# Kernel optimization log

Measured on AMD Instinct MI355X. Metric: run time of the kernel, lower is better.

## Reference

```python
import jax, jax.numpy as jnp
import numpy as np

B, C, INTER, T, H, W = 2, 256, 64, 8, 32, 32


def setup_inputs() -> dict:
    key = jax.random.key(0)
    ks = jax.random.split(key, 4)
    scale_q = 1.0 / np.sqrt(C)
    x = jax.random.normal(ks[0], (B, C, T, H, W), dtype=jnp.float32)
    Wq = jax.random.normal(ks[1], (INTER, C), dtype=jnp.float32) * scale_q
    Wk = jax.random.normal(ks[2], (INTER, C), dtype=jnp.float32) * scale_q
    Wv = jax.random.normal(ks[3], (C, C), dtype=jnp.float32) * scale_q
    return {
        "x": x,
        "Wq": Wq, "bq": jnp.zeros((INTER,), jnp.float32),
        "Wk": Wk, "bk": jnp.zeros((INTER,), jnp.float32),
        "Wv": Wv, "bv": jnp.zeros((C,), jnp.float32),
    }


def reference(x, Wq, bq, Wk, bk, Wv, bv):
    b, c, t, h, w = x.shape
    n = t * h * w
    xf = x.reshape(b, c, n)  # [B, C, N] (row-major flatten over T,H,W)
    # 1x1x1 Conv3d == per-voxel linear projection
    q = jnp.einsum('oc,bcn->bno', Wq, xf) + bq          # [B, N, INTER]
    k = jnp.einsum('oc,bcn->bon', Wk, xf) + bk[:, None]  # [B, INTER, N]
    v = jnp.einsum('oc,bcn->bon', Wv, xf) + bv[:, None]  # [B, C, N]
    energy = jnp.einsum('bid,bdj->bij', q, k)            # [B, N, N]
    attention = jax.nn.softmax(energy, axis=-1)
    # out[b,c,i] = sum_j v[b,c,j] * attention[b,i,j]
    out = jnp.einsum('bcj,bij->bci', v, attention)       # [B, C, N]
    out = out.reshape(b, c, t, h, w) + x
    return out
```

## Files before the change

### kernel.cpp

```cpp
#include <hip/hip_runtime.h>
#include <hip/hip_bf16.h>

typedef short short8 __attribute__((ext_vector_type(8)));
typedef float float4v __attribute__((ext_vector_type(4)));

#define MFMA(a, b, c) __builtin_amdgcn_mfma_f32_16x16x32_bf16((a), (b), (c), 0, 0, 0)

typedef const __attribute__((address_space(1))) unsigned int gu32;
typedef __attribute__((address_space(3))) unsigned int lu32;
#define GLOAD_LDS16(g, l) __builtin_amdgcn_global_load_lds((gu32*)(g), (lu32*)(l), 16, 0, 0)

#define LOG2E 1.4426950408889634f

static __device__ __forceinline__ unsigned short f2bf(float f) {
    union { float f; unsigned u; } v; v.f = f;
    unsigned r = (v.u + 0x7fffu + ((v.u >> 16) & 1u)) >> 16;
    return (unsigned short)r;
}
static __device__ __forceinline__ float bf2f(unsigned short h) {
    union { unsigned u; float f; } v; v.u = ((unsigned)h) << 16;
    return v.f;
}
static __device__ __forceinline__ unsigned pk2bf(float a, float b) {
    union { __hip_bfloat162 h; unsigned u; } cv;
    cv.h = __float22bfloat162_rn(make_float2(a, b));
    return cv.u;
}

static __device__ __forceinline__ int qk_idx(int b, int n, int o) {
    int frag = (b * 512 + (n >> 4)) * 2 + (o >> 5);
    return frag * 512 + ((o >> 3) & 3) * 128 + (n & 15) * 8 + (o & 7);
}
static __device__ __forceinline__ int v_idx(int b, int c, int n) {
    int frag = (b * 256 + (n >> 5)) * 16 + (c >> 4);
    return frag * 512 + ((n >> 3) & 3) * 128 + (c & 15) * 8 + (n & 7);
}

__global__ void wcvt(const float* __restrict__ Wq, const float* __restrict__ Wk,
                     const float* __restrict__ Wv,
                     unsigned short* __restrict__ Whi, unsigned short* __restrict__ Wlo) {
    int idx = blockIdx.x * 256 + threadIdx.x;
    if (idx >= 384 * 256) return;
    int row = idx >> 8, c = idx & 255;
    float f;
    if (row < 64)       f = Wq[row * 256 + c];
    else if (row < 128) f = Wk[(row - 64) * 256 + c];
    else                f = Wv[(row - 128) * 256 + c];
    unsigned short hi = f2bf(f);
    Whi[idx] = hi;
    if (row < 128) Wlo[idx] = f2bf(f - bf2f(hi));
}

__global__ __launch_bounds__(256, 1) void proj(
        const float* __restrict__ x, const unsigned short* __restrict__ Whi,
        const unsigned short* __restrict__ Wlo,
        const float* __restrict__ bq, const float* __restrict__ bk,
        const float* __restrict__ bv,
        unsigned short* __restrict__ qhi_ws, unsigned short* __restrict__ qlo_ws,
        unsigned short* __restrict__ khi_ws, unsigned short* __restrict__ klo_ws,
        unsigned short* __restrict__ vws) {
    __shared__ unsigned short XThi[64 * 264];
    __shared__ unsigned short XTlo[64 * 264];

    const int tid = threadIdx.x;
    const int b  = blockIdx.x >> 7;
    const int n0 = (blockIdx.x & 127) << 6;
    const float* xb = x + b * 2097152;

    for (int p = 0; p < 16; ++p) {
        int idx = p * 256 + tid;
        int c = idx >> 4, nq = idx & 15;
        float4v xv = *reinterpret_cast<const float4v*>(xb + c * 8192 + n0 + nq * 4);
#pragma unroll
        for (int q = 0; q < 4; ++q) {
            unsigned short hi = f2bf(xv[q]);
            XThi[(nq * 4 + q) * 264 + c] = hi;
            XTlo[(nq * 4 + q) * 264 + c] = f2bf(xv[q] - bf2f(hi));
        }
    }
    __syncthreads();

    const int lane = tid & 63, w = tid >> 6;
    const int quad = lane >> 4, l16 = lane & 15;

    short8 aXhi[8], aXlo[8];
#pragma unroll
    for (int ks = 0; ks < 8; ++ks) {
        aXhi[ks] = *reinterpret_cast<const short8*>(&XThi[(w * 16 + l16) * 264 + ks * 32 + quad * 8]);
        aXlo[ks] = *reinterpret_cast<const short8*>(&XTlo[(w * 16 + l16) * 264 + ks * 32 + quad * 8]);
    }

#pragma unroll
    for (int ot = 0; ot < 8; ++ot) {
        float4v acc = {0.f, 0.f, 0.f, 0.f};
#pragma unroll
        for (int ks = 0; ks < 8; ++ks) {
            short8 bwhi = *reinterpret_cast<const short8*>(&Whi[(ot * 16 + l16) * 256 + ks * 32 + quad * 8]);
            short8 bwlo = *reinterpret_cast<const short8*>(&Wlo[(ot * 16 + l16) * 256 + ks * 32 + quad * 8]);
            acc = MFMA(aXhi[ks], bwhi, acc);
            acc = MFMA(aXlo[ks], bwhi, acc);
            acc = MFMA(aXhi[ks], bwlo, acc);
        }
        int o = ot * 16 + l16;
        float bias = (ot < 4) ? bq[o] : bk[o - 64];
#pragma unroll
        for (int r = 0; r < 4; ++r) {
            int n = n0 + w * 16 + quad * 4 + r;
            float y = acc[r] + bias;
            if (ot < 4) y *= LOG2E;
            unsigned short hi = f2bf(y);
            unsigned short lo = f2bf(y - bf2f(hi));
            if (ot < 4) {
                int id = qk_idx(b, n, o);
                qhi_ws[id] = hi; qlo_ws[id] = lo;
            } else {
                int id = qk_idx(b, n, o - 64);
                khi_ws[id] = hi; klo_ws[id] = lo;
            }
        }
    }

    float4v acc2[4][4];
#pragma unroll
    for (int mt = 0; mt < 4; ++mt)
#pragma unroll
        for (int nt = 0; nt < 4; ++nt) acc2[mt][nt] = (float4v){0.f, 0.f, 0.f, 0.f};

#pragma unroll
    for (int ks = 0; ks < 8; ++ks) {
        short8 aW[4], bX[4];
#pragma unroll
        for (int mt = 0; mt < 4; ++mt)
            aW[mt] = *reinterpret_cast<const short8*>(&Whi[(128 + w * 64 + mt * 16 + l16) * 256 + ks * 32 + quad * 8]);
#pragma unroll
        for (int nt = 0; nt < 4; ++nt)
            bX[nt] = *reinterpret_cast<const short8*>(&XThi[(nt * 16 + l16) * 264 + ks * 32 + quad * 8]);
#pragma unroll
        for (int mt = 0; mt < 4; ++mt)
#pragma unroll
            for (int nt = 0; nt < 4; ++nt)
                acc2[mt][nt] = MFMA(aW[mt], bX[nt], acc2[mt][nt]);
    }
#pragma unroll
    for (int mt = 0; mt < 4; ++mt) {
#pragma unroll
        for (int r = 0; r < 4; ++r) {
            int c = w * 64 + mt * 16 + quad * 4 + r;
            float bias = bv[c];
#pragma unroll
            for (int nt = 0; nt < 4; ++nt) {
                int n = n0 + nt * 16 + l16;
                vws[v_idx(b, c, n)] = f2bf(acc2[mt][nt][r] + bias);
            }
        }
    }
}

__global__ __launch_bounds__(256, 2) void attn(
        const unsigned short* __restrict__ qhi_ws, const unsigned short* __restrict__ qlo_ws,
        const unsigned short* __restrict__ khi_ws, const unsigned short* __restrict__ klo_ws,
        const unsigned short* __restrict__ vws,
        unsigned short* __restrict__ Opart, float* __restrict__ ml) {
    __shared__ unsigned short Vlds[3][8192];
    __shared__ unsigned short Pl[4 * 32 * 36];

    const int tid = threadIdx.x, lane = tid & 63, w = tid >> 6;
    const int quad = lane >> 4, l16 = lane & 15;
    const int xcd = blockIdx.x & 7, b = xcd & 1, jr = xcd >> 1;
    const int it = blockIdx.x >> 3;
    const int iw16 = it * 8 + w * 2;
    unsigned short* Pw = Pl + w * (32 * 36);

    const unsigned short* khb = khi_ws + (size_t)((b * 512 + jr * 128) * 2) * 512 + lane * 8;
    const unsigned short* klb = klo_ws + (size_t)((b * 512 + jr * 128) * 2) * 512 + lane * 8;
    const unsigned short* qhb = qhi_ws + (size_t)((b * 512 + iw16) * 2) * 512 + lane * 8;
    const unsigned short* qlb = qlo_ws + (size_t)((b * 512 + iw16) * 2) * 512 + lane * 8;
    const unsigned short* vstage = vws + ((size_t)(b * 256 + jr * 64) * 16 + w * 4) * 512 + lane * 8;

    short8 qh[2][2], ql[2][2];
#pragma unroll
    for (int mt = 0; mt < 2; ++mt)
#pragma unroll
        for (int kf = 0; kf < 2; ++kf) {
            qh[mt][kf] = *reinterpret_cast<const short8*>(qhb + (mt * 2 + kf) * 512);
            ql[mt][kf] = *reinterpret_cast<const short8*>(qlb + (mt * 2 + kf) * 512);
        }

    float4v acc[2][16];
#pragma unroll
    for (int mt = 0; mt < 2; ++mt)
#pragma unroll
        for (int cf = 0; cf < 16; ++cf) acc[mt][cf] = (float4v){0.f, 0.f, 0.f, 0.f};
    float lrow[2][4];
    short8 aP[2];
#pragma unroll
    for (int mt = 0; mt < 2; ++mt)
#pragma unroll
        for (int r = 0; r < 4; ++r) lrow[mt][r] = 0.f;

#pragma unroll
    for (int q = 0; q < 4; ++q)
        GLOAD_LDS16(vstage + q * 512, &Vlds[0][(w * 4 + q) * 512]);
    vstage += 8192;

    int bprev = 2, bcur = 0, bnext = 1;
#pragma unroll 1
    for (int itn = 0; itn < 64; ++itn) {
        if (itn) __syncthreads();

        if (itn < 63) {
#pragma unroll
            for (int q = 0; q < 4; ++q)
                GLOAD_LDS16(vstage + q * 512, &Vlds[bnext][(w * 4 + q) * 512]);
            vstage += 8192;
        }

        float4v s[2][2];
#pragma unroll
        for (int mt = 0; mt < 2; ++mt)
#pragma unroll
            for (int jt = 0; jt < 2; ++jt) s[mt][jt] = (float4v){0.f, 0.f, 0.f, 0.f};
#pragma unroll
        for (int jt = 0; jt < 2; ++jt) {
            short8 kh0 = *reinterpret_cast<const short8*>(khb + (jt * 2 + 0) * 512);
            short8 kh1 = *reinterpret_cast<const short8*>(khb + (jt * 2 + 1) * 512);
            short8 kl0 = *reinterpret_cast<const short8*>(klb + (jt * 2 + 0) * 512);
            short8 kl1 = *reinterpret_cast<const short8*>(klb + (jt * 2 + 1) * 512);
#pragma unroll
            for (int mt = 0; mt < 2; ++mt) {
                s[mt][jt] = MFMA(qh[mt][0], kh0, s[mt][jt]);
                s[mt][jt] = MFMA(ql[mt][0], kh0, s[mt][jt]);
                s[mt][jt] = MFMA(qh[mt][0], kl0, s[mt][jt]);
                s[mt][jt] = MFMA(qh[mt][1], kh1, s[mt][jt]);
                s[mt][jt] = MFMA(ql[mt][1], kh1, s[mt][jt]);
                s[mt][jt] = MFMA(qh[mt][1], kl1, s[mt][jt]);
            }
        }
        khb += 2048; klb += 2048;

        if (itn) {
            const unsigned short* vl = &Vlds[bprev][0];
#pragma unroll
            for (int cf = 0; cf < 16; ++cf) {
                short8 v0 = *reinterpret_cast<const short8*>(vl + cf * 512 + lane * 8);
                acc[0][cf] = MFMA(aP[0], v0, acc[0][cf]);
                acc[1][cf] = MFMA(aP[1], v0, acc[1][cf]);
            }
        }

#pragma unroll
        for (int mt = 0; mt < 2; ++mt)
#pragma unroll
            for (int jt = 0; jt < 2; ++jt) {
                float p0 = exp2f(s[mt][jt][0]);
                float p1 = exp2f(s[mt][jt][1]);
                float p2 = exp2f(s[mt][jt][2]);
                float p3 = exp2f(s[mt][jt][3]);
                lrow[mt][0] += p0; lrow[mt][1] += p1;
                lrow[mt][2] += p2; lrow[mt][3] += p3;
                unsigned u01 = pk2bf(p0, p1);
                unsigned u23 = pk2bf(p2, p3);
                int base = (mt * 16 + quad * 4) * 36 + jt * 16 + l16;
                Pw[base]          = (unsigned short)u01;
                Pw[base + 36]     = (unsigned short)(u01 >> 16);
                Pw[base + 72]     = (unsigned short)u23;
                Pw[base + 108]    = (unsigned short)(u23 >> 16);
            }

#pragma unroll
        for (int mt = 0; mt < 2; ++mt)
            aP[mt] = *reinterpret_cast<const short8*>(&Pw[(mt * 16 + l16) * 36 + quad * 8]);

        int t = bprev; bprev = bcur; bcur = bnext; bnext = t;
    }

    {
        const unsigned short* vl = &Vlds[bprev][0];
#pragma unroll
        for (int cf = 0; cf < 16; ++cf) {
            short8 v0 = *reinterpret_cast<const short8*>(vl + cf * 512 + lane * 8);
            acc[0][cf] = MFMA(aP[0], v0, acc[0][cf]);
            acc[1][cf] = MFMA(aP[1], v0, acc[1][cf]);
        }
    }

#pragma unroll
    for (int mt = 0; mt < 2; ++mt)
#pragma unroll
        for (int r = 0; r < 4; ++r) {
            float lv = lrow[mt][r];
            lv += __shfl_xor(lv, 1);
            lv += __shfl_xor(lv, 2);
            lv += __shfl_xor(lv, 4);
            lv += __shfl_xor(lv, 8);
            if (l16 == 0) {
                int iloc = w * 32 + mt * 16 + quad * 4 + r;
                ml[blockIdx.x * 128 + iloc] = lv;
            }
        }

    unsigned short* ob = Opart + (size_t)blockIdx.x * 32768;
#pragma unroll
    for (int mt = 0; mt < 2; ++mt)
#pragma unroll
        for (int cf = 0; cf < 16; ++cf) {
            unsigned u01 = pk2bf(acc[mt][cf][0], acc[mt][cf][1]);
            unsigned u23 = pk2bf(acc[mt][cf][2], acc[mt][cf][3]);
            int iloc = w * 32 + mt * 16 + quad * 4;
            ob[(iloc + 0) * 256 + cf * 16 + l16] = (unsigned short)u01;
            ob[(iloc + 1) * 256 + cf * 16 + l16] = (unsigned short)(u01 >> 16);
            ob[(iloc + 2) * 256 + cf * 16 + l16] = (unsigned short)u23;
            ob[(iloc + 3) * 256 + cf * 16 + l16] = (unsigned short)(u23 >> 16);
        }
}

__global__ __launch_bounds__(256) void combine(
        const unsigned short* __restrict__ Opart, const float* __restrict__ ml,
        const float* __restrict__ x, float* __restrict__ out) {
    __shared__ float fac[128];
    __shared__ float trans[64 * 130];

    const int t = threadIdx.x;
    const int blk = blockIdx.x;
    const int b = blk & 1, cc = (blk >> 1) & 3, it = blk >> 3;

    if (t < 128) {
        float sum = 0.f;
#pragma unroll
        for (int s = 0; s < 4; ++s)
            sum += ml[(size_t)((it << 3) | (s << 1) | b) * 128 + t];
        fac[t] = 1.0f / sum;
    }
    __syncthreads();

    {
        const int cgrp = t & 7, irow = t >> 3;
#pragma unroll
        for (int ip = 0; ip < 4; ++ip) {
            int i = ip * 32 + irow;
            float a[8];
#pragma unroll
            for (int e = 0; e < 8; ++e) a[e] = 0.f;
#pragma unroll
            for (int s = 0; s < 4; ++s) {
                const unsigned short* op = Opart +
                    (size_t)((it << 3) | (s << 1) | b) * 32768 + i * 256 + cc * 64 + cgrp * 8;
                short8 o = *reinterpret_cast<const short8*>(op);
#pragma unroll
                for (int e = 0; e < 8; ++e) a[e] += bf2f((unsigned short)o[e]);
            }
            float f = fac[i];
#pragma unroll
            for (int e = 0; e < 8; ++e) trans[(cgrp * 8 + e) * 130 + i] = a[e] * f;
        }
    }
    __syncthreads();

    {
        const int c2 = t >> 2, iq = t & 3;
        const int cg = cc * 64 + c2;
        const float* xr = x + (size_t)b * 2097152 + (size_t)cg * 8192 + it * 128;
        float* orow = out + (size_t)b * 2097152 + (size_t)cg * 8192 + it * 128;
#pragma unroll 2
        for (int k = 0; k < 8; ++k) {
            int i = iq * 4 + k * 16;
            float4v o;
#pragma unroll
            for (int r = 0; r < 4; ++r) o[r] = trans[c2 * 130 + i + r];
            float4v xv = *reinterpret_cast<const float4v*>(xr + i);
#pragma unroll
            for (int r = 0; r < 4; ++r) o[r] += xv[r];
            *reinterpret_cast<float4v*>(orow + i) = o;
        }
    }
}

extern "C" void kernel_launch(void* const* d_in, const int* in_sizes, int n_in,
                              void* d_out, int out_size, void* d_ws, size_t ws_size,
                              hipStream_t stream) {
    const float* x  = (const float*)d_in[0];
    const float* Wq = (const float*)d_in[1];
    const float* bq = (const float*)d_in[2];
    const float* Wk = (const float*)d_in[3];
    const float* bk = (const float*)d_in[4];
    const float* Wv = (const float*)d_in[5];
    const float* bv = (const float*)d_in[6];

    unsigned short* Whi = (unsigned short*)d_ws;
    unsigned short* Wlo = Whi + 384 * 256;
    unsigned short* qhi = Wlo + 128 * 256;
    unsigned short* qlo = qhi + 2 * 8192 * 64;
    unsigned short* khi = qlo + 2 * 8192 * 64;
    unsigned short* klo = khi + 2 * 8192 * 64;
    unsigned short* vws = klo + 2 * 8192 * 64;
    unsigned short* Opart = vws + 2 * 256 * 8192;
    float* ml = (float*)(Opart + (size_t)512 * 32768);

    wcvt<<<384, 256, 0, stream>>>(Wq, Wk, Wv, Whi, Wlo);
    proj<<<256, 256, 0, stream>>>(x, Whi, Wlo, bq, bk, bv, qhi, qlo, khi, klo, vws);
    attn<<<512, 256, 0, stream>>>(qhi, qlo, khi, klo, vws, Opart, ml);
    combine<<<512, 256, 0, stream>>>(Opart, ml, x, (float*)d_out);
}
```

Before: 263.5 us.

## Use 8 waves per attention block and stage K tiles through LDS

```diff
diff --git a/kernel.cpp b/kernel.cpp
--- a/kernel.cpp
+++ b/kernel.cpp
@@ -156,52 +156,49 @@
     }
 }
 
-__global__ __launch_bounds__(256, 2) void attn(
+__global__ __launch_bounds__(512, 4) void attn(
         const unsigned short* __restrict__ qhi_ws, const unsigned short* __restrict__ qlo_ws,
         const unsigned short* __restrict__ khi_ws, const unsigned short* __restrict__ klo_ws,
         const unsigned short* __restrict__ vws,
         unsigned short* __restrict__ Opart, float* __restrict__ ml) {
     __shared__ unsigned short Vlds[3][8192];
-    __shared__ unsigned short Pl[4 * 32 * 36];
+    __shared__ unsigned short Klds[2][4096];
+    __shared__ unsigned short Pl[8 * 16 * 36];
 
     const int tid = threadIdx.x, lane = tid & 63, w = tid >> 6;
     const int quad = lane >> 4, l16 = lane & 15;
     const int xcd = blockIdx.x & 7, b = xcd & 1, jr = xcd >> 1;
     const int it = blockIdx.x >> 3;
-    const int iw16 = it * 8 + w * 2;
-    unsigned short* Pw = Pl + w * (32 * 36);
-
-    const unsigned short* khb = khi_ws + (size_t)((b * 512 + jr * 128) * 2) * 512 + lane * 8;
-    const unsigned short* klb = klo_ws + (size_t)((b * 512 + jr * 128) * 2) * 512 + lane * 8;
+    const int iw16 = it * 8 + w;
+    unsigned short* Pw = Pl + w * (16 * 36);
+
     const unsigned short* qhb = qhi_ws + (size_t)((b * 512 + iw16) * 2) * 512 + lane * 8;
     const unsigned short* qlb = qlo_ws + (size_t)((b * 512 + iw16) * 2) * 512 + lane * 8;
-    const unsigned short* vstage = vws + ((size_t)(b * 256 + jr * 64) * 16 + w * 4) * 512 + lane * 8;
-
-    short8 qh[2][2], ql[2][2];
-#pragma unroll
-    for (int mt = 0; mt < 2; ++mt)
-#pragma unroll
-        for (int kf = 0; kf < 2; ++kf) {
-            qh[mt][kf] = *reinterpret_cast<const short8*>(qhb + (mt * 2 + kf) * 512);
-            ql[mt][kf] = *reinterpret_cast<const short8*>(qlb + (mt * 2 + kf) * 512);
-        }
-
-    float4v acc[2][16];
-#pragma unroll
-    for (int mt = 0; mt < 2; ++mt)
-#pragma unroll
-        for (int cf = 0; cf < 16; ++cf) acc[mt][cf] = (float4v){0.f, 0.f, 0.f, 0.f};
-    float lrow[2][4];
-    short8 aP[2];
-#pragma unroll
-    for (int mt = 0; mt < 2; ++mt)
-#pragma unroll
-        for (int r = 0; r < 4; ++r) lrow[mt][r] = 0.f;
-
-#pragma unroll
-    for (int q = 0; q < 4; ++q)
-        GLOAD_LDS16(vstage + q * 512, &Vlds[0][(w * 4 + q) * 512]);
-    vstage += 8192;
+    short8 qh[2], ql[2];
+#pragma unroll
+    for (int kf = 0; kf < 2; ++kf) {
+        qh[kf] = *reinterpret_cast<const short8*>(qhb + kf * 512);
+        ql[kf] = *reinterpret_cast<const short8*>(qlb + kf * 512);
+    }
+
+    const int kw = w & 3;
+    const int koff = ((w & 4) ? 2048 : 0) + kw * 512;
+    const unsigned short* kstage = ((w & 4) ? klo_ws : khi_ws) +
+        (size_t)((b * 512 + jr * 128) * 2) * 512 + kw * 512 + lane * 8;
+    const unsigned short* vstage = vws +
+        (size_t)(b * 256 + jr * 64) * 16 * 512 + w * 512 + lane * 8;
+
+    float4v acc[16];
+#pragma unroll
+    for (int cf = 0; cf < 16; ++cf) acc[cf] = (float4v){0.f, 0.f, 0.f, 0.f};
+    float lrow[4] = {0.f, 0.f, 0.f, 0.f};
+    short8 aP;
+
+    GLOAD_LDS16(kstage, &Klds[0][koff]);
+    GLOAD_LDS16(vstage, &Vlds[0][w * 512]);
+    GLOAD_LDS16(vstage + 4096, &Vlds[0][4096 + w * 512]);
+    kstage += 2048; vstage += 8192;
+    __syncthreads();
 
     int bprev = 2, bcur = 0, bnext = 1;
 #pragma unroll 1
@@ -209,67 +206,57 @@
         if (itn) __syncthreads();
 
         if (itn < 63) {
-#pragma unroll
-            for (int q = 0; q < 4; ++q)
-                GLOAD_LDS16(vstage + q * 512, &Vlds[bnext][(w * 4 + q) * 512]);
-            vstage += 8192;
-        }
-
-        float4v s[2][2];
-#pragma unroll
-        for (int mt = 0; mt < 2; ++mt)
-#pragma unroll
-            for (int jt = 0; jt < 2; ++jt) s[mt][jt] = (float4v){0.f, 0.f, 0.f, 0.f};
+            GLOAD_LDS16(kstage, &Klds[(itn + 1) & 1][koff]);
+            GLOAD_LDS16(vstage, &Vlds[bnext][w * 512]);
+            GLOAD_LDS16(vstage + 4096, &Vlds[bnext][4096 + w * 512]);
+            kstage += 2048; vstage += 8192;
+        }
+
+        const unsigned short* Kc = &Klds[itn & 1][0];
+        float4v s[2];
+        s[0] = (float4v){0.f, 0.f, 0.f, 0.f};
+        s[1] = (float4v){0.f, 0.f, 0.f, 0.f};
 #pragma unroll
         for (int jt = 0; jt < 2; ++jt) {
-            short8 kh0 = *reinterpret_cast<const short8*>(khb + (jt * 2 + 0) * 512);
-            short8 kh1 = *reinterpret_cast<const short8*>(khb + (jt * 2 + 1) * 512);
-            short8 kl0 = *reinterpret_cast<const short8*>(klb + (jt * 2 + 0) * 512);
-            short8 kl1 = *reinterpret_cast<const short8*>(klb + (jt * 2 + 1) * 512);
-#pragma unroll
-            for (int mt = 0; mt < 2; ++mt) {
-                s[mt][jt] = MFMA(qh[mt][0], kh0, s[mt][jt]);
-                s[mt][jt] = MFMA(ql[mt][0], kh0, s[mt][jt]);
-                s[mt][jt] = MFMA(qh[mt][0], kl0, s[mt][jt]);
-                s[mt][jt] = MFMA(qh[mt][1], kh1, s[mt][jt]);
-                s[mt][jt] = MFMA(ql[mt][1], kh1, s[mt][jt]);
-                s[mt][jt] = MFMA(qh[mt][1], kl1, s[mt][jt]);
-            }
-        }
-        khb += 2048; klb += 2048;
+            short8 kh0 = *reinterpret_cast<const short8*>(Kc + (jt * 2 + 0) * 512 + lane * 8);
+            short8 kh1 = *reinterpret_cast<const short8*>(Kc + (jt * 2 + 1) * 512 + lane * 8);
+            short8 kl0 = *reinterpret_cast<const short8*>(Kc + 2048 + (jt * 2 + 0) * 512 + lane * 8);
+            short8 kl1 = *reinterpret_cast<const short8*>(Kc + 2048 + (jt * 2 + 1) * 512 + lane * 8);
+            s[jt] = MFMA(qh[0], kh0, s[jt]);
+            s[jt] = MFMA(ql[0], kh0, s[jt]);
+            s[jt] = MFMA(qh[0], kl0, s[jt]);
+            s[jt] = MFMA(qh[1], kh1, s[jt]);
+            s[jt] = MFMA(ql[1], kh1, s[jt]);
+            s[jt] = MFMA(qh[1], kl1, s[jt]);
+        }
 
         if (itn) {
             const unsigned short* vl = &Vlds[bprev][0];
 #pragma unroll
             for (int cf = 0; cf < 16; ++cf) {
                 short8 v0 = *reinterpret_cast<const short8*>(vl + cf * 512 + lane * 8);
-                acc[0][cf] = MFMA(aP[0], v0, acc[0][cf]);
-                acc[1][cf] = MFMA(aP[1], v0, acc[1][cf]);
+                acc[cf] = MFMA(aP, v0, acc[cf]);
             }
         }
 
 #pragma unroll
-        for (int mt = 0; mt < 2; ++mt)
-#pragma unroll
-            for (int jt = 0; jt < 2; ++jt) {
-                float p0 = exp2f(s[mt][jt][0]);
-                float p1 = exp2f(s[mt][jt][1]);
-                float p2 = exp2f(s[mt][jt][2]);
-                float p3 = exp2f(s[mt][jt][3]);
-                lrow[mt][0] += p0; lrow[mt][1] += p1;
-                lrow[mt][2] += p2; lrow[mt][3] += p3;
-                unsigned u01 = pk2bf(p0, p1);
-                unsigned u23 = pk2bf(p2, p3);
-                int base = (mt * 16 + quad * 4) * 36 + jt * 16 + l16;
-                Pw[base]          = (unsigned short)u01;
-                Pw[base + 36]     = (unsigned short)(u01 >> 16);
-                Pw[base + 72]     = (unsigned short)u23;
-                Pw[base + 108]    = (unsigned short)(u23 >> 16);
-            }
-
-#pragma unroll
-        for (int mt = 0; mt < 2; ++mt)
-            aP[mt] = *reinterpret_cast<const short8*>(&Pw[(mt * 16 + l16) * 36 + quad * 8]);
+        for (int jt = 0; jt < 2; ++jt) {
+            float p0 = exp2f(s[jt][0]);
+            float p1 = exp2f(s[jt][1]);
+            float p2 = exp2f(s[jt][2]);
+            float p3 = exp2f(s[jt][3]);
+            lrow[0] += p0; lrow[1] += p1;
+            lrow[2] += p2; lrow[3] += p3;
+            unsigned u01 = pk2bf(p0, p1);
+            unsigned u23 = pk2bf(p2, p3);
+            int base = (quad * 4) * 36 + jt * 16 + l16;
+            Pw[base]       = (unsigned short)u01;
+            Pw[base + 36]  = (unsigned short)(u01 >> 16);
+            Pw[base + 72]  = (unsigned short)u23;
+            Pw[base + 108] = (unsigned short)(u23 >> 16);
+        }
+
+        aP = *reinterpret_cast<const short8*>(&Pw[l16 * 36 + quad * 8]);
 
         int t = bprev; bprev = bcur; bcur = bnext; bnext = t;
     }
@@ -279,39 +266,32 @@
 #pragma unroll
         for (int cf = 0; cf < 16; ++cf) {
             short8 v0 = *reinterpret_cast<const short8*>(vl + cf * 512 + lane * 8);
-            acc[0][cf] = MFMA(aP[0], v0, acc[0][cf]);
-            acc[1][cf] = MFMA(aP[1], v0, acc[1][cf]);
-        }
-    }
-
-#pragma unroll
-    for (int mt = 0; mt < 2; ++mt)
-#pragma unroll
-        for (int r = 0; r < 4; ++r) {
-            float lv = lrow[mt][r];
-            lv += __shfl_xor(lv, 1);
-            lv += __shfl_xor(lv, 2);
-            lv += __shfl_xor(lv, 4);
-            lv += __shfl_xor(lv, 8);
-            if (l16 == 0) {
-                int iloc = w * 32 + mt * 16 + quad * 4 + r;
-                ml[blockIdx.x * 128 + iloc] = lv;
-            }
-        }
+            acc[cf] = MFMA(aP, v0, acc[cf]);
+        }
+    }
+
+#pragma unroll
+    for (int r = 0; r < 4; ++r) {
+        float lv = lrow[r];
+        lv += __shfl_xor(lv, 1);
+        lv += __shfl_xor(lv, 2);
+        lv += __shfl_xor(lv, 4);
+        lv += __shfl_xor(lv, 8);
+        if (l16 == 0)
+            ml[blockIdx.x * 128 + w * 16 + quad * 4 + r] = lv;
+    }
 
     unsigned short* ob = Opart + (size_t)blockIdx.x * 32768;
 #pragma unroll
-    for (int mt = 0; mt < 2; ++mt)
-#pragma unroll
-        for (int cf = 0; cf < 16; ++cf) {
-            unsigned u01 = pk2bf(acc[mt][cf][0], acc[mt][cf][1]);
-            unsigned u23 = pk2bf(acc[mt][cf][2], acc[mt][cf][3]);
-            int iloc = w * 32 + mt * 16 + quad * 4;
-            ob[(iloc + 0) * 256 + cf * 16 + l16] = (unsigned short)u01;
-            ob[(iloc + 1) * 256 + cf * 16 + l16] = (unsigned short)(u01 >> 16);
-            ob[(iloc + 2) * 256 + cf * 16 + l16] = (unsigned short)u23;
-            ob[(iloc + 3) * 256 + cf * 16 + l16] = (unsigned short)(u23 >> 16);
-        }
+    for (int cf = 0; cf < 16; ++cf) {
+        unsigned u01 = pk2bf(acc[cf][0], acc[cf][1]);
+        unsigned u23 = pk2bf(acc[cf][2], acc[cf][3]);
+        int iloc = w * 16 + quad * 4;
+        ob[(iloc + 0) * 256 + cf * 16 + l16] = (unsigned short)u01;
+        ob[(iloc + 1) * 256 + cf * 16 + l16] = (unsigned short)(u01 >> 16);
+        ob[(iloc + 2) * 256 + cf * 16 + l16] = (unsigned short)u23;
+        ob[(iloc + 3) * 256 + cf * 16 + l16] = (unsigned short)(u23 >> 16);
+    }
 }
 
 __global__ __launch_bounds__(256) void combine(
@@ -398,6 +378,6 @@
 
     wcvt<<<384, 256, 0, stream>>>(Wq, Wk, Wv, Whi, Wlo);
     proj<<<256, 256, 0, stream>>>(x, Whi, Wlo, bq, bk, bv, qhi, qlo, khi, klo, vws);
-    attn<<<512, 256, 0, stream>>>(qhi, qlo, khi, klo, vws, Opart, ml);
+    attn<<<512, 512, 0, stream>>>(qhi, qlo, khi, klo, vws, Opart, ml);
     combine<<<512, 256, 0, stream>>>(Opart, ml, x, (float*)d_out);
 }
```

New measurement: 245.3 us. 6.9% less time.
